# Kernel tuning notes

Hardware: AMD Instinct MI355X
Metric: run time of the kernel (lower is better)

Reference implementation:

```python
import jax, jax.numpy as jnp
import numpy as np

PI = float(np.pi)


def _layernorm(x, g, b, eps=1e-5):
    mu = jnp.mean(x, axis=-1, keepdims=True)
    var = jnp.var(x, axis=-1, keepdims=True)
    return (x - mu) * jax.lax.rsqrt(var + eps) * g + b


def setup_inputs() -> dict:
    key = jax.random.key(0)
    B, L, D, P = 4, 2048, 256, 32
    ks = jax.random.split(key, 16)

    def lin_w(k, fi, fo):
        return (jax.random.normal(k, (fi, fo), dtype=jnp.float32) / np.sqrt(fi)).astype(jnp.float32)

    inp = {
        'x': jax.random.normal(ks[0], (B, L, D), dtype=jnp.float32),
        'pos_phases': jax.random.normal(ks[1], (L, P), dtype=jnp.float32) * PI,
        'w_mem1v': lin_w(ks[2], D, P), 'b_mem1v': jnp.zeros((P,), jnp.float32),
        'w_mem1o': lin_w(ks[3], P, D), 'b_mem1o': jnp.zeros((D,), jnp.float32),
        'w_off': lin_w(ks[4], D + P, P), 'b_off': jnp.zeros((P,), jnp.float32),
        'w_key': lin_w(ks[5], D, P), 'b_key': jnp.zeros((P,), jnp.float32),
        'w_val': lin_w(ks[6], D, D), 'b_val': jnp.zeros((D,), jnp.float32),
        'w_sk1': lin_w(ks[7], 2 * D, D), 'b_sk1': jnp.zeros((D,), jnp.float32),
        'w_sk2': lin_w(ks[8], D, P), 'b_sk2': jnp.zeros((P,), jnp.float32),
        'w_gate': lin_w(ks[9], D, 1), 'b_gate': jnp.zeros((1,), jnp.float32),
        'ln_g': jnp.ones((D,), jnp.float32), 'ln_b': jnp.zeros((D,), jnp.float32),
        'w_out': lin_w(ks[10], D, D), 'b_out': jnp.zeros((D,), jnp.float32),
    }
    return inp


def reference(x, pos_phases, w_mem1v, b_mem1v, w_mem1o, b_mem1o, w_off, b_off,
              w_key, b_key, w_val, b_val, w_sk1, b_sk1, w_sk2, b_sk2,
              w_gate, b_gate, ln_g, ln_b, w_out, b_out):
    B, L, D = x.shape
    P = pos_phases.shape[-1]

    pos_cos = jnp.cos(pos_phases)  # [L,P]
    pos_sin = jnp.sin(pos_phases)

    # Memory 1: flat [B,L,P] phasor cumulative memory
    v1 = x @ w_mem1v + b_mem1v                       # [B,L,P]
    mem1_cos = jnp.cumsum(pos_cos[None] * v1, axis=1)
    mem1_sin = jnp.cumsum(pos_sin[None] * v1, axis=1)

    offset_input = jnp.concatenate([x, jnp.broadcast_to(pos_phases[None], (B, L, P))], axis=-1)
    offset = jnp.tanh(offset_input @ w_off + b_off) * PI
    oc, os = jnp.cos(offset), jnp.sin(offset)
    query_cos = pos_cos[None] * oc - pos_sin[None] * os
    query_sin = pos_sin[None] * oc + pos_cos[None] * os
    pos_ret = (mem1_cos * query_cos + mem1_sin * query_sin) / np.sqrt(P)
    pos_out = pos_ret @ w_mem1o + b_mem1o            # [B,L,D]

    # Memory 2: full [B,L,P,D] phasor KV cumulative memory
    key_phases = jnp.tanh(x @ w_key + b_key) * PI    # [B,L,P]
    key_cos, key_sin = jnp.cos(key_phases), jnp.sin(key_phases)
    values = x @ w_val + b_val                       # [B,L,D]
    store_gate = jax.nn.sigmoid(x @ w_gate + b_gate) # [B,L,1]

    positions = jnp.arange(1, L + 1, dtype=x.dtype)[None, :, None]
    context_avg = jnp.cumsum(x, axis=1) / positions
    h = jax.nn.gelu(jnp.concatenate([x, context_avg], axis=-1) @ w_sk1 + b_sk1, approximate=False)
    storage_phases = jnp.tanh(h @ w_sk2 + b_sk2) * PI  # [B,L,P]

    gated_v = values * store_gate                    # [B,L,D]
    kv_mem_cos = jnp.cumsum(jnp.cos(storage_phases)[..., None] * gated_v[:, :, None, :], axis=1)  # [B,L,P,D]
    kv_mem_sin = jnp.cumsum(jnp.sin(storage_phases)[..., None] * gated_v[:, :, None, :], axis=1)

    gate_cumsum = jnp.clip(jnp.cumsum(store_gate, axis=1), 1.0, None)  # [B,L,1]
    kv_retrieved = jnp.einsum('blpd,blp->bld', kv_mem_cos, key_cos) + \
                   jnp.einsum('blpd,blp->bld', kv_mem_sin, key_sin)
    kv_retrieved = kv_retrieved / (jnp.sqrt(gate_cumsum) * np.sqrt(P))

    combined = pos_out + kv_retrieved
    return x + _layernorm(combined, ln_g, ln_b) @ w_out + b_out
```

## Files before the change

kernel.cpp:

```cpp
#include <hip/hip_runtime.h>
#include <hip/hip_bf16.h>

constexpr int B_ = 4;
constexpr int L_ = 2048;
constexpr int D_ = 256;
constexpr int P_ = 32;
constexpr int CL = 32;
constexpr int NC = L_ / CL;

#define PI_F 3.14159265358979323846f
#define INV_SQRT_P 0.17677669529663687f

typedef __attribute__((ext_vector_type(8))) short short8_t;
typedef __attribute__((ext_vector_type(4))) float floatx4;

static __device__ inline short f2bf(float f) {
  unsigned int u;
  __builtin_memcpy(&u, &f, 4);
  unsigned int r = (u + 0x7fffu + ((u >> 16) & 1u)) >> 16;
  return (short)r;
}
static __device__ inline float bf2f(short s) {
  unsigned int u = ((unsigned int)(unsigned short)s) << 16;
  float f;
  __builtin_memcpy(&f, &u, 4);
  return f;
}

__global__ void wprep(const float* __restrict__ x, const float* __restrict__ pos,
                      const float* __restrict__ w_val, const float* __restrict__ w_mem1v,
                      const float* __restrict__ w_off, const float* __restrict__ b_off,
                      const float* __restrict__ w_key, const float* __restrict__ w_gate,
                      const float* __restrict__ w_sk1, const float* __restrict__ w_out,
                      const float* __restrict__ w_sk2, const float* __restrict__ w_mem1o,
                      short* __restrict__ WA, short* __restrict__ W1,
                      short* __restrict__ WO, short* __restrict__ W2T,
                      short* __restrict__ W1OT,
                      short* __restrict__ xbf, float* __restrict__ poff,
                      float* __restrict__ ctxsum) {
  __shared__ float2 psum[2][128];
  int blk = blockIdx.x, tid = threadIdx.x;
  if (blk < 384) {
    int idx = blk * 256 + tid;
    int n = idx >> 8, k = idx & 255;
    float v;
    if (n < 256) v = w_val[k * 256 + n];
    else if (n < 288) v = w_mem1v[k * 32 + (n - 256)];
    else if (n < 320) v = w_off[k * 32 + (n - 288)];
    else if (n < 352) v = w_key[k * 32 + (n - 320)];
    else if (n == 352) v = w_gate[k];
    else v = 0.f;
    WA[idx] = f2bf(v);
  } else if (blk < 896) {
    int idx = (blk - 384) * 256 + tid;
    int n = idx >> 9, k = idx & 511;
    W1[idx] = f2bf(w_sk1[k * 256 + n]);
  } else if (blk < 1152) {
    int idx = (blk - 896) * 256 + tid;
    int n = idx >> 8, k = idx & 255;
    WO[idx] = f2bf(w_out[k * 256 + n]);
  } else if (blk < 1184) {
    int idx = (blk - 1152) * 256 + tid;
    int p = idx >> 8, k = idx & 255;
    W2T[idx] = f2bf(w_sk2[k * 32 + p]);
  } else if (blk < 1216) {
    int idx = (blk - 1184) * 256 + tid;
    int d = idx >> 5, p = idx & 31;
    W1OT[idx] = f2bf(w_mem1o[p * 256 + d]);
  } else if (blk < 1472) {
    int idx = (blk - 1216) * 256 + tid;
    int l = idx >> 5, p = idx & 31;
    float a = b_off[p];
#pragma unroll 8
    for (int j = 0; j < 32; ++j) a += pos[l * 32 + j] * w_off[(256 + j) * 32 + p];
    poff[idx] = a;
  } else {
    int c2 = blk - 1472;
    int b = c2 >> 6, ch = c2 & 63;
    int d2 = (tid & 127) * 2, h = tid >> 7;
    int tokb = b * L_ + ch * 32 + h * 16;
    float2 xv[16];
#pragma unroll
    for (int i = 0; i < 16; ++i)
      xv[i] = *(const float2*)&x[(tokb + i) * 256 + d2];
    float2 s = {0.f, 0.f};
#pragma unroll
    for (int i = 0; i < 16; ++i) { s.x += xv[i].x; s.y += xv[i].y; }
#pragma unroll
    for (int i = 0; i < 16; ++i) {
      short2 o;
      o.x = f2bf(xv[i].x);
      o.y = f2bf(xv[i].y);
      *(short2*)&xbf[(tokb + i) * 256 + d2] = o;
    }
    psum[h][tid & 127] = s;
    __syncthreads();
    if (h == 0) {
      float2 o = psum[1][tid & 127];
      float2 tot = {s.x + o.x, s.y + o.y};
      *(float2*)&ctxsum[c2 * 256 + d2] = tot;
    }
  }
}

__global__ __launch_bounds__(768, 6) void gemmA3(const short* __restrict__ xbf,
                                                 const short* __restrict__ WA,
                                                 const float* __restrict__ pos,
                                                 const float* __restrict__ poff,
                                                 const float* __restrict__ b_mem1v,
                                                 const float* __restrict__ b_key,
                                                 const float* __restrict__ b_gate,
                                                 const float* __restrict__ b_val,
                                                 float* __restrict__ m1cT,
                                                 float* __restrict__ m1sT,
                                                 float* __restrict__ qc,
                                                 float* __restrict__ qs,
                                                 short* __restrict__ K2bf,
                                                 short* __restrict__ gvT,
                                                 float* __restrict__ sg,
                                                 float* __restrict__ ctxsum) {
  __shared__ float YL[16][132];
  __shared__ float gsh[16];
  int tid = threadIdx.x;
  int bc = blockIdx.x;
  if (bc >= 512) {
    if (tid < 256) {
      int b = bc - 512;
      int base = b * 64 * 256 + tid;
      float run = 0.f;
      for (int c0 = 0; c0 < 64; c0 += 8) {
        float v[8];
#pragma unroll
        for (int j = 0; j < 8; ++j) v[j] = ctxsum[base + (c0 + j) * 256];
#pragma unroll
        for (int j = 0; j < 8; ++j) {
          ctxsum[base + (c0 + j) * 256] = run;
          run += v[j];
        }
      }
    }
    return;
  }
  int lane = tid & 63, w = tid >> 6;
  int ml = lane & 15, quad = lane >> 4, kq = quad * 8;
  int bc32 = bc >> 1, half = bc & 1;
  int tok0 = bc * 16;
  float posv = 0.f, poffv = 0.f;
  if (tid < 512) {
    int t = tid >> 5, p = tid & 31;
    int l = (tok0 + t) & (L_ - 1);
    posv = pos[l * 32 + p];
    poffv = poff[l * 32 + p];
  }
  floatx4 acc[2] = {};
  const short* A0p = &xbf[(tok0 + ml) * 256 + kq];
  const short* Bp = &WA[(w * 32 + ml) * 256 + kq];
#pragma unroll
  for (int ks = 0; ks < 8; ++ks) {
    short8_t a0 = *(const short8_t*)(A0p + ks * 32);
#pragma unroll
    for (int nt = 0; nt < 2; ++nt) {
      short8_t b = *(const short8_t*)(Bp + nt * 16 * 256 + ks * 32);
      acc[nt] = __builtin_amdgcn_mfma_f32_16x16x32_bf16(a0, b, acc[nt], 0, 0, 0);
    }
  }
  if (w >= 8) {
#pragma unroll
    for (int nt = 0; nt < 2; ++nt) {
      int col = (w - 8) * 32 + nt * 16 + ml;
#pragma unroll
      for (int r = 0; r < 4; ++r)
        YL[quad * 4 + r][col] = acc[nt][r];
    }
  }
  __syncthreads();
  if (tid < 512) {
    int t = tid >> 5, p = tid & 31;
    int tok = tok0 + t, l = tok & (L_ - 1);
    int b = tok >> 11;
    float v1 = YL[t][p] + b_mem1v[p];
    float pc = cosf(posv), ps = sinf(posv);
    int idxT = (b * 32 + p) * L_ + l;
    m1cT[idxT] = pc * v1;
    m1sT[idxT] = ps * v1;
    float off = tanhf(YL[t][32 + p] + poffv) * PI_F;
    float oc = cosf(off), os = sinf(off);
    int gidx = tok * 32 + p;
    qc[gidx] = pc * oc - ps * os;
    qs[gidx] = ps * oc + pc * os;
    float kp = tanhf(YL[t][64 + p] + b_key[p]) * PI_F;
    K2bf[tok * 64 + p] = f2bf(cosf(kp));
    K2bf[tok * 64 + 32 + p] = f2bf(sinf(kp));
    if (p == 0) {
      float g = 1.f / (1.f + expf(-(YL[t][96] + b_gate[0])));
      sg[tok] = g;
      gsh[t] = g;
    }
  }
  __syncthreads();
  if (w < 8) {
#pragma unroll
    for (int nt = 0; nt < 2; ++nt) {
      int d = w * 32 + nt * 16 + ml;
      float bv = b_val[d];
      int t0 = quad * 4;
      short4 o;
      o.x = f2bf((acc[nt][0] + bv) * gsh[t0 + 0]);
      o.y = f2bf((acc[nt][1] + bv) * gsh[t0 + 1]);
      o.z = f2bf((acc[nt][2] + bv) * gsh[t0 + 2]);
      o.w = f2bf((acc[nt][3] + bv) * gsh[t0 + 3]);
      *(short4*)&gvT[(bc32 * 256 + d) * 32 + half * 16 + t0] = o;
    }
  }
}

union __align__(16) CDMem {
  short As[32][520];
  struct { short HS[32][280]; short SPL[64][40]; } h;
};
__global__ __launch_bounds__(1024, 4) void gemmCD(const short* __restrict__ xbf,
                                                  const float* __restrict__ x,
                                                  const float* __restrict__ ctxsum,
                                                  const short* __restrict__ W1,
                                                  const float* __restrict__ b_sk1,
                                                  const short* __restrict__ W2T,
                                                  const float* __restrict__ b_sk2,
                                                  const short* __restrict__ gvT,
                                                  short* __restrict__ SPbf,
                                                  short* __restrict__ UT) {
  __shared__ CDMem sm;
  __shared__ float stmp[4][256];
  int tid = threadIdx.x;
  int bc = blockIdx.x;
  int tok0 = bc * 32;
  int bI = bc >> 6, ch = bc & 63;
  int lane = tid & 63, w = tid >> 6;
  int ml = lane & 15, quad = lane >> 4, kq = quad * 8;
  short8_t bgv = *(const short8_t*)&gvT[(bc * 256 + w * 16 + ml) * 32 + kq];
  {
    int row = tid >> 5, c8 = tid & 31;
    *(short8_t*)&sm.As[row][c8 * 8] =
        *(const short8_t*)&xbf[(tok0 + row) * 256 + c8 * 8];
  }
  {
    int d = tid & 255, qh = tid >> 8;
    float cp = ctxsum[(bI * 64 + ch) * 256 + d];
    float xv[8];
    int xb = (tok0 + qh * 8) * 256 + d;
#pragma unroll
    for (int i = 0; i < 8; ++i) xv[i] = x[xb + i * 256];
    float p = 0.f;
#pragma unroll
    for (int i = 0; i < 8; ++i) p += xv[i];
    stmp[qh][d] = p;
    __syncthreads();
    float run = cp;
    for (int j = 0; j < qh; ++j) run += stmp[j][d];
    int l0 = ch * 32 + qh * 8;
#pragma unroll
    for (int i = 0; i < 8; ++i) {
      run += xv[i];
      sm.As[qh * 8 + i][256 + d] = f2bf(run / (float)(l0 + i + 1));
    }
  }
  __syncthreads();
  int n0w = w * 16;
  floatx4 acc[2] = {};
#pragma unroll
  for (int kt = 0; kt < 16; ++kt) {
    short8_t a0 = *(short8_t*)&sm.As[ml][kt * 32 + kq];
    short8_t a1 = *(short8_t*)&sm.As[16 + ml][kt * 32 + kq];
    short8_t b0 = *(const short8_t*)&W1[(n0w + ml) * 512 + kt * 32 + kq];
    acc[0] = __builtin_amdgcn_mfma_f32_16x16x32_bf16(a0, b0, acc[0], 0, 0, 0);
    acc[1] = __builtin_amdgcn_mfma_f32_16x16x32_bf16(a1, b0, acc[1], 0, 0, 0);
  }
  short hv[2][4];
  {
    float bv = b_sk1[n0w + ml];
#pragma unroll
    for (int mt = 0; mt < 2; ++mt)
#pragma unroll
      for (int r = 0; r < 4; ++r) {
        float v = acc[mt][r] + bv;
        float g = 0.5f * v * (1.f + erff(v * 0.70710678118654752f));
        hv[mt][r] = f2bf(g);
      }
  }
  __syncthreads();
#pragma unroll
  for (int mt = 0; mt < 2; ++mt)
#pragma unroll
    for (int r = 0; r < 4; ++r)
      sm.h.HS[mt * 16 + quad * 4 + r][n0w + ml] = hv[mt][r];
  __syncthreads();
  if (w < 4) {
    int th = w & 1, ph = w >> 1;
    floatx4 pacc = {};
#pragma unroll
    for (int s = 0; s < 8; ++s) {
      short8_t a = *(short8_t*)&sm.h.HS[th * 16 + ml][s * 32 + kq];
      short8_t b0 = *(const short8_t*)&W2T[(ph * 16 + ml) * 256 + s * 32 + kq];
      pacc = __builtin_amdgcn_mfma_f32_16x16x32_bf16(a, b0, pacc, 0, 0, 0);
    }
    int p = ph * 16 + ml;
    float bs = b_sk2[p];
#pragma unroll
    for (int r = 0; r < 4; ++r) {
      int tl = th * 16 + quad * 4 + r;
      int tok = tok0 + tl;
      float sp = tanhf(pacc[r] + bs) * PI_F;
      short c = f2bf(cosf(sp)), s2 = f2bf(sinf(sp));
      sm.h.SPL[p][tl] = c;
      sm.h.SPL[32 + p][tl] = s2;
      SPbf[tok * 64 + p] = c;
      SPbf[tok * 64 + 32 + p] = s2;
    }
  }
  __syncthreads();
  short8_t a[4];
#pragma unroll
  for (int mt = 0; mt < 4; ++mt) a[mt] = *(short8_t*)&sm.h.SPL[mt * 16 + ml][kq];
  floatx4 acc3[4] = {};
#pragma unroll
  for (int mt = 0; mt < 4; ++mt)
    acc3[mt] = __builtin_amdgcn_mfma_f32_16x16x32_bf16(a[mt], bgv, acc3[mt], 0, 0, 0);
#pragma unroll
  for (int mt = 0; mt < 4; ++mt) {
    int d = w * 16 + ml;
    short4 o;
    o.x = f2bf(acc3[mt][0]);
    o.y = f2bf(acc3[mt][1]);
    o.z = f2bf(acc3[mt][2]);
    o.w = f2bf(acc3[mt][3]);
    *(short4*)&UT[(bc * 256 + d) * 64 + mt * 16 + quad * 4] = o;
  }
}

__global__ void scanE(float* __restrict__ m1cT, float* __restrict__ m1sT,
                      float* __restrict__ sg, short* __restrict__ UT) {
  __shared__ float wsum[4];
  __shared__ float stot[4][64];
  int blk = blockIdx.x;
  int tid = threadIdx.x;
  if (blk >= 260) {
    int eb = blk - 260;
    int w = tid >> 6, lane = tid & 63;
    int pi = eb * 64 + lane;
    int q = pi & 63;
    int d = (pi >> 6) & 255;
    int b = pi >> 14;
    const int cs = 256 * 64;
    int base = ((b * NC) * 256 + d) * 64 + q;
    short v[16];
#pragma unroll
    for (int c = 0; c < 16; ++c) v[c] = UT[base + (w * 16 + c) * cs];
    float tot = 0.f;
#pragma unroll
    for (int c = 0; c < 16; ++c) tot += bf2f(v[c]);
    stot[w][lane] = tot;
    __syncthreads();
    float run = 0.f;
    for (int ww = 0; ww < w; ++ww) run += stot[ww][lane];
#pragma unroll
    for (int c = 0; c < 16; ++c) {
      UT[base + (w * 16 + c) * cs] = f2bf(run);
      run += bf2f(v[c]);
    }
    return;
  }
  int lane = tid & 63, w = tid >> 6;
  float* arr;
  int base;
  if (blk < 256) {
    arr = (blk < 128) ? m1cT : m1sT;
    base = (blk & 127) * L_;
  } else {
    arr = sg;
    base = (blk - 256) * L_;
  }
  int sbase = base + w * 512;
  float v[8];
#pragma unroll
  for (int i = 0; i < 8; ++i) v[i] = arr[sbase + i * 64 + lane];
  float carry = 0.f;
#pragma unroll
  for (int i = 0; i < 8; ++i) {
    float vv = v[i];
#pragma unroll
    for (int off = 1; off < 64; off <<= 1) {
      float n = __shfl_up(vv, off, 64);
      if (lane >= off) vv += n;
    }
    vv += carry;
    v[i] = vv;
    carry = __shfl(vv, 63, 64);
  }
  if (lane == 0) wsum[w] = carry;
  __syncthreads();
  float off = 0.f;
  for (int ww = 0; ww < w; ++ww) off += wsum[ww];
#pragma unroll
  for (int i = 0; i < 8; ++i) arr[sbase + i * 64 + lane] = v[i] + off;
}

struct __align__(16) FGMem {
  short SL[32][40];
  short PR[32][40];
  float CMB[32][260];
  short CBN[32][280];
  float LG[256], LB[256];
  float scl[32], mu_s[32], rs_s[32];
};
__global__ __launch_bounds__(1024, 4) void fgOut(const short* __restrict__ UT,
                                                 const short* __restrict__ SPbf,
                                                 const short* __restrict__ K2bf,
                                                 const short* __restrict__ gvT,
                                                 const float* __restrict__ sgc,
                                                 const float* __restrict__ m1cT,
                                                 const float* __restrict__ m1sT,
                                                 const float* __restrict__ qc,
                                                 const float* __restrict__ qs,
                                                 const short* __restrict__ W1OT,
                                                 const float* __restrict__ b_mem1o,
                                                 const float* __restrict__ ln_g,
                                                 const float* __restrict__ ln_b,
                                                 const short* __restrict__ WO,
                                                 const float* __restrict__ b_out,
                                                 const float* __restrict__ x,
                                                 float* __restrict__ out) {
  __shared__ FGMem sm;
  int tid5 = threadIdx.x;
  int bc = blockIdx.x;
  int lbase = bc * CL;
  int bb = bc >> 6, lloc = (bc & 63) * 32;
  int lane = tid5 & 63, w = tid5 >> 6;
  int ml = lane & 15, quad = lane >> 4, kq = quad * 8;
  int d0 = w * 16;
  short8_t ub0 = *(const short8_t*)&UT[(bc * 256 + d0 + ml) * 64 + kq];
  short8_t ub1 = *(const short8_t*)&UT[(bc * 256 + d0 + ml) * 64 + 32 + kq];
  short8_t gvb = *(const short8_t*)&gvT[(bc * 256 + d0 + ml) * 32 + kq];
  short8_t w1b = *(const short8_t*)&W1OT[(d0 + ml) * 32 + kq];
  const float4* x4 = (const float4*)&x[lbase * 256];
  float4 xp0 = x4[tid5];
  float4 xp1 = x4[tid5 + 1024];
  if (tid5 < 32) sm.scl[tid5] = rsqrtf(fmaxf(sgc[lbase + tid5], 1.f)) * INV_SQRT_P;
  if (tid5 >= 256 && tid5 < 512) {
    int d = tid5 - 256;
    sm.LG[d] = ln_g[d];
    sm.LB[d] = ln_b[d];
  }
  short8_t ka0 = *(const short8_t*)&K2bf[(lbase + ml) * 64 + kq];
  short8_t ka1 = *(const short8_t*)&K2bf[(lbase + 16 + ml) * 64 + kq];
  short8_t kb0 = *(const short8_t*)&K2bf[(lbase + ml) * 64 + 32 + kq];
  short8_t kb1 = *(const short8_t*)&K2bf[(lbase + 16 + ml) * 64 + 32 + kq];
  if (w == 0) {
    floatx4 sacc[2][2] = {};
#pragma unroll
    for (int ks2 = 0; ks2 < 2; ++ks2) {
      short8_t a0 = (ks2 == 0) ? ka0 : kb0;
      short8_t a1 = (ks2 == 0) ? ka1 : kb1;
      short8_t b0 = *(const short8_t*)&SPbf[(lbase + ml) * 64 + ks2 * 32 + kq];
      short8_t b1 = *(const short8_t*)&SPbf[(lbase + 16 + ml) * 64 + ks2 * 32 + kq];
      sacc[0][0] = __builtin_amdgcn_mfma_f32_16x16x32_bf16(a0, b0, sacc[0][0], 0, 0, 0);
      sacc[0][1] = __builtin_amdgcn_mfma_f32_16x16x32_bf16(a0, b1, sacc[0][1], 0, 0, 0);
      sacc[1][0] = __builtin_amdgcn_mfma_f32_16x16x32_bf16(a1, b0, sacc[1][0], 0, 0, 0);
      sacc[1][1] = __builtin_amdgcn_mfma_f32_16x16x32_bf16(a1, b1, sacc[1][1], 0, 0, 0);
    }
#pragma unroll
    for (int mt = 0; mt < 2; ++mt)
#pragma unroll
      for (int nt = 0; nt < 2; ++nt)
#pragma unroll
        for (int r = 0; r < 4; ++r) {
          int trow = mt * 16 + quad * 4 + r;
          int scol = nt * 16 + ml;
          float v = (scol <= trow) ? sacc[mt][nt][r] : 0.f;
          sm.SL[trow][scol] = f2bf(v);
        }
  } else {
    int t7 = tid5 - 64;
    for (int i = t7; i < 1024; i += 960) {
      int pp = i >> 5, t = i & 31;
      int gT = (bb * 32 + pp) * L_ + lloc + t;
      int g = (lbase + t) * 32 + pp;
      sm.PR[t][pp] = f2bf((m1cT[gT] * qc[g] + m1sT[gT] * qs[g]) * INV_SQRT_P);
    }
  }
  __syncthreads();
  floatx4 acc[2] = {};
  acc[0] = __builtin_amdgcn_mfma_f32_16x16x32_bf16(ka0, ub0, acc[0], 0, 0, 0);
  acc[1] = __builtin_amdgcn_mfma_f32_16x16x32_bf16(ka1, ub0, acc[1], 0, 0, 0);
  acc[0] = __builtin_amdgcn_mfma_f32_16x16x32_bf16(kb0, ub1, acc[0], 0, 0, 0);
  acc[1] = __builtin_amdgcn_mfma_f32_16x16x32_bf16(kb1, ub1, acc[1], 0, 0, 0);
  {
    short8_t a0 = *(short8_t*)&sm.SL[ml][kq];
    short8_t a1 = *(short8_t*)&sm.SL[16 + ml][kq];
    acc[0] = __builtin_amdgcn_mfma_f32_16x16x32_bf16(a0, gvb, acc[0], 0, 0, 0);
    acc[1] = __builtin_amdgcn_mfma_f32_16x16x32_bf16(a1, gvb, acc[1], 0, 0, 0);
  }
  floatx4 macc[2] = {};
  {
    short8_t a0 = *(short8_t*)&sm.PR[ml][kq];
    short8_t a1 = *(short8_t*)&sm.PR[16 + ml][kq];
    macc[0] = __builtin_amdgcn_mfma_f32_16x16x32_bf16(a0, w1b, macc[0], 0, 0, 0);
    macc[1] = __builtin_amdgcn_mfma_f32_16x16x32_bf16(a1, w1b, macc[1], 0, 0, 0);
  }
  {
    int d = d0 + ml;
    float bm = b_mem1o[d];
#pragma unroll
    for (int mt = 0; mt < 2; ++mt)
#pragma unroll
      for (int r = 0; r < 4; ++r) {
        int t = mt * 16 + quad * 4 + r;
        sm.CMB[t][d] = acc[mt][r] * sm.scl[t] + macc[mt][r] + bm;
      }
  }
  __syncthreads();
  {
    int t = tid5 >> 5, g = tid5 & 31;
    float s = 0.f, s2 = 0.f;
#pragma unroll
    for (int j = 0; j < 8; ++j) {
      float v = sm.CMB[t][g + j * 32];
      s += v;
      s2 += v * v;
    }
#pragma unroll
    for (int m = 1; m < 32; m <<= 1) {
      s += __shfl_xor(s, m, 64);
      s2 += __shfl_xor(s2, m, 64);
    }
    if (g == 0) {
      float mu = s / (float)D_;
      float var = s2 / (float)D_ - mu * mu;
      sm.mu_s[t] = mu;
      sm.rs_s[t] = rsqrtf(var + 1e-5f);
    }
  }
  __syncthreads();
#pragma unroll
  for (int it = 0; it < 8; ++it) {
    int i = it * 1024 + tid5;
    int t = i >> 8, d = i & 255;
    sm.CBN[t][d] = f2bf((sm.CMB[t][d] - sm.mu_s[t]) * sm.rs_s[t] * sm.LG[d] + sm.LB[d]);
  }
  __syncthreads();
  floatx4 acc2[2] = {};
#pragma unroll
  for (int kt = 0; kt < 8; ++kt) {
    short8_t a0 = *(short8_t*)&sm.CBN[ml][kt * 32 + kq];
    short8_t a1 = *(short8_t*)&sm.CBN[16 + ml][kt * 32 + kq];
    short8_t b = *(const short8_t*)&WO[(d0 + ml) * 256 + kt * 32 + kq];
    acc2[0] = __builtin_amdgcn_mfma_f32_16x16x32_bf16(a0, b, acc2[0], 0, 0, 0);
    acc2[1] = __builtin_amdgcn_mfma_f32_16x16x32_bf16(a1, b, acc2[1], 0, 0, 0);
  }
  {
    int n = d0 + ml;
    float bv = b_out[n];
#pragma unroll
    for (int mt = 0; mt < 2; ++mt)
#pragma unroll
      for (int r = 0; r < 4; ++r) {
        int t = mt * 16 + quad * 4 + r;
        sm.CMB[t][n] = acc2[mt][r] + bv;
      }
  }
  __syncthreads();
  {
    float4* o4 = (float4*)&out[lbase * 256];
#pragma unroll
    for (int k = 0; k < 2; ++k) {
      int idx4 = tid5 + k * 1024;
      int t = idx4 >> 6, dd = (idx4 & 63) * 4;
      float4 xp = (k == 0) ? xp0 : xp1;
      float4 o;
      o.x = xp.x + sm.CMB[t][dd + 0];
      o.y = xp.y + sm.CMB[t][dd + 1];
      o.z = xp.z + sm.CMB[t][dd + 2];
      o.w = xp.w + sm.CMB[t][dd + 3];
      o4[idx4] = o;
    }
  }
}

extern "C" void kernel_launch(void* const* d_in, const int* in_sizes, int n_in,
                              void* d_out, int out_size, void* d_ws, size_t ws_size,
                              hipStream_t stream) {
  const float* x = (const float*)d_in[0];
  const float* pos = (const float*)d_in[1];
  const float* w_mem1v = (const float*)d_in[2];
  const float* b_mem1v = (const float*)d_in[3];
  const float* w_mem1o = (const float*)d_in[4];
  const float* b_mem1o = (const float*)d_in[5];
  const float* w_off = (const float*)d_in[6];
  const float* b_off = (const float*)d_in[7];
  const float* w_key = (const float*)d_in[8];
  const float* b_key = (const float*)d_in[9];
  const float* w_val = (const float*)d_in[10];
  const float* b_val = (const float*)d_in[11];
  const float* w_sk1 = (const float*)d_in[12];
  const float* b_sk1 = (const float*)d_in[13];
  const float* w_sk2 = (const float*)d_in[14];
  const float* b_sk2 = (const float*)d_in[15];
  const float* w_gate = (const float*)d_in[16];
  const float* b_gate = (const float*)d_in[17];
  const float* ln_g = (const float*)d_in[18];
  const float* ln_b = (const float*)d_in[19];
  const float* w_out = (const float*)d_in[20];
  const float* b_out = (const float*)d_in[21];
  float* out = (float*)d_out;
  float* ws = (float*)d_ws;

  const int BLP = B_ * L_ * P_;
  const int BLD = B_ * L_ * D_;
  float* m1cT = ws;
  float* m1sT = m1cT + BLP;
  float* qc = m1sT + BLP;
  float* qs = qc + BLP;
  float* sg = qs + BLP;
  float* poff = sg + B_ * L_;
  float* ctxsum = poff + L_ * P_;
  short* UT = (short*)(ctxsum + B_ * 64 * 256);
  short* xbf = UT + (size_t)B_ * NC * 256 * 64;
  short* ctxbf = xbf + BLD;
  short* hs = ctxbf + BLD;
  short* gvT = hs + BLD;
  short* K2bf = gvT + BLD;
  short* SPbf = K2bf + B_ * L_ * 64;
  short* WA = SPbf + B_ * L_ * 64;
  short* W1 = WA + 384 * 256;
  short* WO = W1 + 256 * 512;
  short* W2T = WO + 256 * 256;
  short* W1OT = W2T + 32 * 256;

  wprep<<<1728, 256, 0, stream>>>(x, pos, w_val, w_mem1v, w_off, b_off, w_key, w_gate,
                                  w_sk1, w_out, w_sk2, w_mem1o, WA, W1, WO, W2T, W1OT,
                                  xbf, poff, ctxsum);
  gemmA3<<<516, 768, 0, stream>>>(xbf, WA, pos, poff, b_mem1v, b_key, b_gate, b_val,
                                  m1cT, m1sT, qc, qs, K2bf, gvT, sg, ctxsum);
  gemmCD<<<256, 1024, 0, stream>>>(xbf, x, ctxsum, W1, b_sk1, W2T, b_sk2, gvT, SPbf, UT);
  scanE<<<1284, 256, 0, stream>>>(m1cT, m1sT, sg, UT);
  fgOut<<<256, 1024, 0, stream>>>(UT, SPbf, K2bf, gvT, sg, m1cT, m1sT, qc, qs,
                                  W1OT, b_mem1o, ln_g, ln_b, WO, b_out, x, out);
}
```

Baseline: 160.7 us.

## Fuse gemmA3 and gemmCD into one launch with split block roles

Merges the two GEMM kernels into one 512-block launch. Even blocks compute the mem1/offset/key/gate projections and their phasor outputs. Odd blocks recompute the gate and the value projection locally, keep gated values in shared memory for the storage-phase GEMM, and build the chunk-prefix of context sums by looping over earlier chunk sums instead of relying on a separate scan pass. This removes one kernel launch, the global round-trip of gvT between kernels and the serial ctxsum scan blocks. In exchange it adds redundant gate GEMM work, O(chunk) prefix reads per block, and load imbalance between the two block roles.

```diff
diff --git a/kernel.cpp b/kernel.cpp
--- a/kernel.cpp
+++ b/kernel.cpp
@@ -103,176 +103,152 @@
   }
 }
 
-__global__ __launch_bounds__(768, 6) void gemmA3(const short* __restrict__ xbf,
-                                                 const short* __restrict__ WA,
-                                                 const float* __restrict__ pos,
-                                                 const float* __restrict__ poff,
-                                                 const float* __restrict__ b_mem1v,
-                                                 const float* __restrict__ b_key,
-                                                 const float* __restrict__ b_gate,
-                                                 const float* __restrict__ b_val,
-                                                 float* __restrict__ m1cT,
-                                                 float* __restrict__ m1sT,
-                                                 float* __restrict__ qc,
-                                                 float* __restrict__ qs,
-                                                 short* __restrict__ K2bf,
-                                                 short* __restrict__ gvT,
-                                                 float* __restrict__ sg,
-                                                 float* __restrict__ ctxsum) {
-  __shared__ float YL[16][132];
-  __shared__ float gsh[16];
+union __align__(16) ACDMem {
+  float YL[32][132];
+  struct { short As[32][520]; float stmp[4][256]; float cpsh[256]; } s;
+  struct { short HS[32][280]; short SPL[64][40]; short GV[256][40]; } h;
+};
+__global__ __launch_bounds__(1024, 4) void a3cd(
+    const short* __restrict__ xbf, const float* __restrict__ x,
+    const float* __restrict__ ctxsum, const short* __restrict__ WA,
+    const short* __restrict__ W1, const short* __restrict__ W2T,
+    const float* __restrict__ pos, const float* __restrict__ poff,
+    const float* __restrict__ b_mem1v, const float* __restrict__ b_key,
+    const float* __restrict__ b_gate, const float* __restrict__ b_val,
+    const float* __restrict__ b_sk1, const float* __restrict__ b_sk2,
+    float* __restrict__ m1cT, float* __restrict__ m1sT,
+    float* __restrict__ qc, float* __restrict__ qs,
+    short* __restrict__ K2bf, float* __restrict__ sg,
+    short* __restrict__ gvT, short* __restrict__ SPbf,
+    short* __restrict__ UT) {
+  __shared__ ACDMem sm;
+  __shared__ float gshc[32];
   int tid = threadIdx.x;
-  int bc = blockIdx.x;
-  if (bc >= 512) {
-    if (tid < 256) {
-      int b = bc - 512;
-      int base = b * 64 * 256 + tid;
-      float run = 0.f;
-      for (int c0 = 0; c0 < 64; c0 += 8) {
-        float v[8];
-#pragma unroll
-        for (int j = 0; j < 8; ++j) v[j] = ctxsum[base + (c0 + j) * 256];
-#pragma unroll
-        for (int j = 0; j < 8; ++j) {
-          ctxsum[base + (c0 + j) * 256] = run;
-          run += v[j];
-        }
-      }
-    }
-    return;
-  }
   int lane = tid & 63, w = tid >> 6;
   int ml = lane & 15, quad = lane >> 4, kq = quad * 8;
-  int bc32 = bc >> 1, half = bc & 1;
-  int tok0 = bc * 16;
-  float posv = 0.f, poffv = 0.f;
-  if (tid < 512) {
+  int bc = blockIdx.x;
+  int cn = bc >> 1;
+  int tok0 = cn * 32;
+  if ((bc & 1) == 0) {
+    int th = w & 1, cg = w >> 1;
     int t = tid >> 5, p = tid & 31;
-    int l = (tok0 + t) & (L_ - 1);
-    posv = pos[l * 32 + p];
-    poffv = poff[l * 32 + p];
-  }
-  floatx4 acc[2] = {};
-  const short* A0p = &xbf[(tok0 + ml) * 256 + kq];
-  const short* Bp = &WA[(w * 32 + ml) * 256 + kq];
-#pragma unroll
-  for (int ks = 0; ks < 8; ++ks) {
-    short8_t a0 = *(const short8_t*)(A0p + ks * 32);
-#pragma unroll
-    for (int nt = 0; nt < 2; ++nt) {
-      short8_t b = *(const short8_t*)(Bp + nt * 16 * 256 + ks * 32);
-      acc[nt] = __builtin_amdgcn_mfma_f32_16x16x32_bf16(a0, b, acc[nt], 0, 0, 0);
-    }
-  }
-  if (w >= 8) {
-#pragma unroll
-    for (int nt = 0; nt < 2; ++nt) {
-      int col = (w - 8) * 32 + nt * 16 + ml;
-#pragma unroll
-      for (int r = 0; r < 4; ++r)
-        YL[quad * 4 + r][col] = acc[nt][r];
-    }
-  }
-  __syncthreads();
-  if (tid < 512) {
-    int t = tid >> 5, p = tid & 31;
-    int tok = tok0 + t, l = tok & (L_ - 1);
-    int b = tok >> 11;
-    float v1 = YL[t][p] + b_mem1v[p];
+    int tok = tok0 + t, l = tok & (L_ - 1), b = tok >> 11;
+    float posv = pos[l * 32 + p];
+    float poffv = poff[l * 32 + p];
+    floatx4 acc = {};
+    const short* Ap = &xbf[(tok0 + th * 16 + ml) * 256 + kq];
+    const short* Bp = &WA[(256 + cg * 16 + ml) * 256 + kq];
+#pragma unroll
+    for (int ks = 0; ks < 8; ++ks) {
+      short8_t a = *(const short8_t*)(Ap + ks * 32);
+      short8_t bb = *(const short8_t*)(Bp + ks * 32);
+      acc = __builtin_amdgcn_mfma_f32_16x16x32_bf16(a, bb, acc, 0, 0, 0);
+    }
+#pragma unroll
+    for (int r = 0; r < 4; ++r)
+      sm.YL[th * 16 + quad * 4 + r][cg * 16 + ml] = acc[r];
+    __syncthreads();
+    float v1 = sm.YL[t][p] + b_mem1v[p];
     float pc = cosf(posv), ps = sinf(posv);
     int idxT = (b * 32 + p) * L_ + l;
     m1cT[idxT] = pc * v1;
     m1sT[idxT] = ps * v1;
-    float off = tanhf(YL[t][32 + p] + poffv) * PI_F;
+    float off = tanhf(sm.YL[t][32 + p] + poffv) * PI_F;
     float oc = cosf(off), os = sinf(off);
     int gidx = tok * 32 + p;
     qc[gidx] = pc * oc - ps * os;
     qs[gidx] = ps * oc + pc * os;
-    float kp = tanhf(YL[t][64 + p] + b_key[p]) * PI_F;
+    float kp = tanhf(sm.YL[t][64 + p] + b_key[p]) * PI_F;
     K2bf[tok * 64 + p] = f2bf(cosf(kp));
     K2bf[tok * 64 + 32 + p] = f2bf(sinf(kp));
     if (p == 0) {
-      float g = 1.f / (1.f + expf(-(YL[t][96] + b_gate[0])));
+      float g = 1.f / (1.f + expf(-(sm.YL[t][96] + b_gate[0])));
       sg[tok] = g;
-      gsh[t] = g;
-    }
-  }
-  __syncthreads();
-  if (w < 8) {
-#pragma unroll
-    for (int nt = 0; nt < 2; ++nt) {
-      int d = w * 32 + nt * 16 + ml;
-      float bv = b_val[d];
-      int t0 = quad * 4;
-      short4 o;
-      o.x = f2bf((acc[nt][0] + bv) * gsh[t0 + 0]);
-      o.y = f2bf((acc[nt][1] + bv) * gsh[t0 + 1]);
-      o.z = f2bf((acc[nt][2] + bv) * gsh[t0 + 2]);
-      o.w = f2bf((acc[nt][3] + bv) * gsh[t0 + 3]);
-      *(short4*)&gvT[(bc32 * 256 + d) * 32 + half * 16 + t0] = o;
-    }
-  }
-}
-
-union __align__(16) CDMem {
-  short As[32][520];
-  struct { short HS[32][280]; short SPL[64][40]; } h;
-};
-__global__ __launch_bounds__(1024, 4) void gemmCD(const short* __restrict__ xbf,
-                                                  const float* __restrict__ x,
-                                                  const float* __restrict__ ctxsum,
-                                                  const short* __restrict__ W1,
-                                                  const float* __restrict__ b_sk1,
-                                                  const short* __restrict__ W2T,
-                                                  const float* __restrict__ b_sk2,
-                                                  const short* __restrict__ gvT,
-                                                  short* __restrict__ SPbf,
-                                                  short* __restrict__ UT) {
-  __shared__ CDMem sm;
-  __shared__ float stmp[4][256];
-  int tid = threadIdx.x;
-  int bc = blockIdx.x;
-  int tok0 = bc * 32;
-  int bI = bc >> 6, ch = bc & 63;
-  int lane = tid & 63, w = tid >> 6;
-  int ml = lane & 15, quad = lane >> 4, kq = quad * 8;
-  short8_t bgv = *(const short8_t*)&gvT[(bc * 256 + w * 16 + ml) * 32 + kq];
+    }
+    return;
+  }
+  int bI = cn >> 6, ch = cn & 63;
   {
     int row = tid >> 5, c8 = tid & 31;
-    *(short8_t*)&sm.As[row][c8 * 8] =
+    *(short8_t*)&sm.s.As[row][c8 * 8] =
         *(const short8_t*)&xbf[(tok0 + row) * 256 + c8 * 8];
   }
   {
     int d = tid & 255, qh = tid >> 8;
-    float cp = ctxsum[(bI * 64 + ch) * 256 + d];
+    if (qh == 0) {
+      float cp = 0.f;
+      int sb = bI * 64 * 256 + d;
+      int c = 0;
+      for (; c + 8 <= ch; c += 8) {
+        float u0 = ctxsum[sb + (c + 0) * 256];
+        float u1 = ctxsum[sb + (c + 1) * 256];
+        float u2 = ctxsum[sb + (c + 2) * 256];
+        float u3 = ctxsum[sb + (c + 3) * 256];
+        float u4 = ctxsum[sb + (c + 4) * 256];
+        float u5 = ctxsum[sb + (c + 5) * 256];
+        float u6 = ctxsum[sb + (c + 6) * 256];
+        float u7 = ctxsum[sb + (c + 7) * 256];
+        cp += ((u0 + u1) + (u2 + u3)) + ((u4 + u5) + (u6 + u7));
+      }
+      for (; c < ch; ++c) cp += ctxsum[sb + c * 256];
+      sm.s.cpsh[d] = cp;
+    }
     float xv[8];
     int xb = (tok0 + qh * 8) * 256 + d;
 #pragma unroll
     for (int i = 0; i < 8; ++i) xv[i] = x[xb + i * 256];
-    float p = 0.f;
-#pragma unroll
-    for (int i = 0; i < 8; ++i) p += xv[i];
-    stmp[qh][d] = p;
+    float pq = 0.f;
+#pragma unroll
+    for (int i = 0; i < 8; ++i) pq += xv[i];
+    sm.s.stmp[qh][d] = pq;
     __syncthreads();
-    float run = cp;
-    for (int j = 0; j < qh; ++j) run += stmp[j][d];
+    float run = sm.s.cpsh[d];
+    for (int j = 0; j < qh; ++j) run += sm.s.stmp[j][d];
     int l0 = ch * 32 + qh * 8;
 #pragma unroll
     for (int i = 0; i < 8; ++i) {
       run += xv[i];
-      sm.As[qh * 8 + i][256 + d] = f2bf(run / (float)(l0 + i + 1));
+      sm.s.As[qh * 8 + i][256 + d] = f2bf(run / (float)(l0 + i + 1));
     }
   }
   __syncthreads();
   int n0w = w * 16;
-  floatx4 acc[2] = {};
+  floatx4 hacc[2] = {};
 #pragma unroll
   for (int kt = 0; kt < 16; ++kt) {
-    short8_t a0 = *(short8_t*)&sm.As[ml][kt * 32 + kq];
-    short8_t a1 = *(short8_t*)&sm.As[16 + ml][kt * 32 + kq];
+    short8_t a0 = *(short8_t*)&sm.s.As[ml][kt * 32 + kq];
+    short8_t a1 = *(short8_t*)&sm.s.As[16 + ml][kt * 32 + kq];
     short8_t b0 = *(const short8_t*)&W1[(n0w + ml) * 512 + kt * 32 + kq];
-    acc[0] = __builtin_amdgcn_mfma_f32_16x16x32_bf16(a0, b0, acc[0], 0, 0, 0);
-    acc[1] = __builtin_amdgcn_mfma_f32_16x16x32_bf16(a1, b0, acc[1], 0, 0, 0);
+    hacc[0] = __builtin_amdgcn_mfma_f32_16x16x32_bf16(a0, b0, hacc[0], 0, 0, 0);
+    hacc[1] = __builtin_amdgcn_mfma_f32_16x16x32_bf16(a1, b0, hacc[1], 0, 0, 0);
+  }
+  floatx4 vacc[2] = {};
+#pragma unroll
+  for (int kt = 0; kt < 8; ++kt) {
+    short8_t a0 = *(short8_t*)&sm.s.As[ml][kt * 32 + kq];
+    short8_t a1 = *(short8_t*)&sm.s.As[16 + ml][kt * 32 + kq];
+    short8_t b0 = *(const short8_t*)&WA[(n0w + ml) * 256 + kt * 32 + kq];
+    vacc[0] = __builtin_amdgcn_mfma_f32_16x16x32_bf16(a0, b0, vacc[0], 0, 0, 0);
+    vacc[1] = __builtin_amdgcn_mfma_f32_16x16x32_bf16(a1, b0, vacc[1], 0, 0, 0);
+  }
+  if (w == 15) {
+    floatx4 gacc[2] = {};
+#pragma unroll
+    for (int kt = 0; kt < 8; ++kt) {
+      short8_t a0 = *(short8_t*)&sm.s.As[ml][kt * 32 + kq];
+      short8_t a1 = *(short8_t*)&sm.s.As[16 + ml][kt * 32 + kq];
+      short8_t b0 = *(const short8_t*)&WA[(352 + ml) * 256 + kt * 32 + kq];
+      gacc[0] = __builtin_amdgcn_mfma_f32_16x16x32_bf16(a0, b0, gacc[0], 0, 0, 0);
+      gacc[1] = __builtin_amdgcn_mfma_f32_16x16x32_bf16(a1, b0, gacc[1], 0, 0, 0);
+    }
+    if (ml == 0) {
+#pragma unroll
+      for (int mt = 0; mt < 2; ++mt)
+#pragma unroll
+        for (int r = 0; r < 4; ++r)
+          gshc[mt * 16 + quad * 4 + r] =
+              1.f / (1.f + expf(-(gacc[mt][r] + b_gate[0])));
+    }
   }
   short hv[2][4];
   {
@@ -281,7 +257,7 @@
     for (int mt = 0; mt < 2; ++mt)
 #pragma unroll
       for (int r = 0; r < 4; ++r) {
-        float v = acc[mt][r] + bv;
+        float v = hacc[mt][r] + bv;
         float g = 0.5f * v * (1.f + erff(v * 0.70710678118654752f));
         hv[mt][r] = f2bf(g);
       }
@@ -292,6 +268,21 @@
 #pragma unroll
     for (int r = 0; r < 4; ++r)
       sm.h.HS[mt * 16 + quad * 4 + r][n0w + ml] = hv[mt][r];
+  {
+    int d = n0w + ml;
+    float bv = b_val[d];
+#pragma unroll
+    for (int mt = 0; mt < 2; ++mt) {
+      int t0 = mt * 16 + quad * 4;
+      short4 o;
+      o.x = f2bf((vacc[mt][0] + bv) * gshc[t0 + 0]);
+      o.y = f2bf((vacc[mt][1] + bv) * gshc[t0 + 1]);
+      o.z = f2bf((vacc[mt][2] + bv) * gshc[t0 + 2]);
+      o.w = f2bf((vacc[mt][3] + bv) * gshc[t0 + 3]);
+      *(short4*)&sm.h.GV[d][t0] = o;
+      *(short4*)&gvT[(cn * 256 + d) * 32 + t0] = o;
+    }
+  }
   __syncthreads();
   if (w < 4) {
     int th = w & 1, ph = w >> 1;
@@ -320,19 +311,20 @@
   short8_t a[4];
 #pragma unroll
   for (int mt = 0; mt < 4; ++mt) a[mt] = *(short8_t*)&sm.h.SPL[mt * 16 + ml][kq];
+  short8_t bgv = *(short8_t*)&sm.h.GV[n0w + ml][kq];
   floatx4 acc3[4] = {};
 #pragma unroll
   for (int mt = 0; mt < 4; ++mt)
     acc3[mt] = __builtin_amdgcn_mfma_f32_16x16x32_bf16(a[mt], bgv, acc3[mt], 0, 0, 0);
 #pragma unroll
   for (int mt = 0; mt < 4; ++mt) {
-    int d = w * 16 + ml;
+    int d = n0w + ml;
     short4 o;
     o.x = f2bf(acc3[mt][0]);
     o.y = f2bf(acc3[mt][1]);
     o.z = f2bf(acc3[mt][2]);
     o.w = f2bf(acc3[mt][3]);
-    *(short4*)&UT[(bc * 256 + d) * 64 + mt * 16 + quad * 4] = o;
+    *(short4*)&UT[(cn * 256 + d) * 64 + mt * 16 + quad * 4] = o;
   }
 }
 
@@ -637,9 +629,9 @@
   wprep<<<1728, 256, 0, stream>>>(x, pos, w_val, w_mem1v, w_off, b_off, w_key, w_gate,
                                   w_sk1, w_out, w_sk2, w_mem1o, WA, W1, WO, W2T, W1OT,
                                   xbf, poff, ctxsum);
-  gemmA3<<<516, 768, 0, stream>>>(xbf, WA, pos, poff, b_mem1v, b_key, b_gate, b_val,
-                                  m1cT, m1sT, qc, qs, K2bf, gvT, sg, ctxsum);
-  gemmCD<<<256, 1024, 0, stream>>>(xbf, x, ctxsum, W1, b_sk1, W2T, b_sk2, gvT, SPbf, UT);
+  a3cd<<<512, 1024, 0, stream>>>(xbf, x, ctxsum, WA, W1, W2T, pos, poff,
+                                 b_mem1v, b_key, b_gate, b_val, b_sk1, b_sk2,
+                                 m1cT, m1sT, qc, qs, K2bf, sg, gvT, SPbf, UT);
   scanE<<<1284, 256, 0, stream>>>(m1cT, m1sT, sg, UT);
   fgOut<<<256, 1024, 0, stream>>>(UT, SPbf, K2bf, gvT, sg, m1cT, m1sT, qc, qs,
                                   W1OT, b_mem1o, ln_g, ln_b, WO, b_out, x, out);
```

New measurement: 167.4 us. +4.2%, slower.
